# Optimization experiments

Measured on AMD Instinct MI355X. Metric: run time of the kernel, lower is better.

The kernel has to match this reference:

```python
import jax, jax.numpy as jnp
import numpy as np

HEADS = 4
HEAD_DIM = 32
DIM = 256
HIDDEN = HEADS * HEAD_DIM  # 128
SCALE = HEAD_DIM ** -0.5


def rmsnorm(x, g):
    # channel-wise L2 normalize (dim=1) * g * sqrt(C), lucidrains-style RMSNorm for conv maps
    inv = jax.lax.rsqrt(jnp.sum(x * x, axis=1, keepdims=True) + 1e-12)
    return x * inv * (g * (x.shape[1] ** 0.5))[None, :, None, None]


def setup_inputs() -> dict:
    key = jax.random.key(0)
    k1, k2, k3 = jax.random.split(key, 3)
    b, H, W = 16, 64, 64
    x = jax.random.normal(k1, (b, DIM, H, W), dtype=jnp.float32)
    W_qkv = jax.random.normal(k2, (3 * HIDDEN, DIM), dtype=jnp.float32) * (DIM ** -0.5)
    W_out = jax.random.normal(k3, (DIM, HIDDEN), dtype=jnp.float32) * (HIDDEN ** -0.5)
    b_out = jnp.zeros((DIM,), dtype=jnp.float32)
    g_norm = jnp.ones((DIM,), dtype=jnp.float32)
    g_out = jnp.ones((DIM,), dtype=jnp.float32)
    return {"x": x, "W_qkv": W_qkv, "W_out": W_out, "b_out": b_out,
            "g_norm": g_norm, "g_out": g_out}


def reference(x, W_qkv, W_out, b_out, g_norm, g_out):
    b, c, H, W = x.shape
    n = H * W
    xn = rmsnorm(x, g_norm)
    # 1x1 conv projection to q,k,v: (b, 3*hidden, H, W)
    qkv = jnp.einsum('bchw,oc->bohw', xn, W_qkv)
    qkv = qkv.reshape(b, 3, HEADS, HEAD_DIM, n)
    q, k, v = qkv[:, 0], qkv[:, 1], qkv[:, 2]  # (b, h, d, n)
    q = jax.nn.softmax(q, axis=-2)  # over head_dim
    k = jax.nn.softmax(k, axis=-1)  # over tokens
    # context: (b, h, d, e)
    context = jnp.einsum('bhdn,bhen->bhde', k, v)
    out = jnp.einsum('bhde,bhdn->bhen', context, q) * SCALE  # (b, h, e, n)
    out = out.reshape(b, HIDDEN, H, W)
    out = jnp.einsum('bchw,oc->bohw', out, W_out) + b_out[None, :, None, None]
    return rmsnorm(out, g_out)
```

## Files before the change

### kernel.cpp

```cpp
#include <hip/hip_runtime.h>


typedef _Float16 half8 __attribute__((ext_vector_type(8)));
typedef _Float16 half4 __attribute__((ext_vector_type(4)));
typedef float f32x4 __attribute__((ext_vector_type(4)));

#define SCALE_F 0.17677669529663687f

__global__ __launch_bounds__(256) void kW(const float* __restrict__ W_qkv,
                                          const float* __restrict__ W_out,
                                          const float* __restrict__ g_norm,
                                          _Float16* __restrict__ W16,
                                          _Float16* __restrict__ Wo16) {
  const int t = threadIdx.x;
  __shared__ float g16s[256];
  g16s[t] = g_norm[t] * 16.0f;
  __syncthreads();
  #pragma unroll
  for (int i = 0; i < 8; ++i) {
    int idx = blockIdx.x * 2048 + i * 256 + t;
    if (idx < 24576) {
      f32x4 v = *(const f32x4*)(W_qkv + (size_t)idx * 4);
      int c0 = (idx & 63) * 4;
      half4 h = {(_Float16)(v[0] * g16s[c0]), (_Float16)(v[1] * g16s[c0 + 1]),
                 (_Float16)(v[2] * g16s[c0 + 2]), (_Float16)(v[3] * g16s[c0 + 3])};
      *(half4*)(W16 + (size_t)idx * 4) = h;
    } else {
      f32x4 v = *(const f32x4*)(W_out + (size_t)(idx - 24576) * 4);
      half4 h = {(_Float16)v[0], (_Float16)v[1], (_Float16)v[2], (_Float16)v[3]};
      *(half4*)(Wo16 + (size_t)(idx - 24576) * 4) = h;
    }
  }
}

#define LOAD_AF(dst, mtv)                                                            \
  {                                                                                  \
    const _Float16* Wm_ = W16 + (size_t)((mtv) * 128 + h * 32) * 256;                \
    _Pragma("unroll")                                                                \
    for (int ks = 0; ks < 8; ++ks)                                                   \
      _Pragma("unroll")                                                              \
      for (int mf = 0; mf < 2; ++mf)                                                 \
        dst[ks][mf] = *(const half8*)(Wm_ + (size_t)(mf * 16 + ll) * 256 +           \
                                      ks * 32 + lg * 8);                             \
  }

#define GEMM_PHASE(afc)                                                              \
  {                                                                                  \
    _Pragma("unroll")                                                                \
    for (int i = 0; i < 2; ++i)                                                      \
      _Pragma("unroll")                                                              \
      for (int j = 0; j < 4; ++j) acc[i][j] = fz;                                    \
    _Pragma("unroll")                                                                \
    for (int ks = 0; ks < 8; ++ks) {                                                 \
      half8 bf[4];                                                                   \
      _Pragma("unroll")                                                              \
      for (int nf = 0; nf < 4; ++nf)                                                 \
        bf[nf] = *(const half8*)(xbuf + (nf * 16 + ll) * 512 +                       \
                                 ((((ks * 4 + lg) ^ ll) ^ ((nf & 1) << 4)) << 4));   \
      _Pragma("unroll")                                                              \
      for (int mf = 0; mf < 2; ++mf)                                                 \
        _Pragma("unroll")                                                            \
        for (int nf = 0; nf < 4; ++nf)                                               \
          acc[mf][nf] =                                                              \
              __builtin_amdgcn_mfma_f32_16x16x32_f16(afc[ks][mf], bf[nf],            \
                                                     acc[mf][nf], 0, 0, 0);          \
    }                                                                                \
  }

__global__ __launch_bounds__(256, 3) void k2_mega(const _Float16* __restrict__ W16,
                                                  const float* __restrict__ x,
                                                  _Float16* __restrict__ qhat,
                                                  float* __restrict__ ctxp,
                                                  float* __restrict__ sumep) {
  const int pt = blockIdx.x, b = blockIdx.y;
  const int p0 = pt * 64;
  const int t = threadIdx.x;
  const int h = t >> 6, l = t & 63;
  const int lg = l >> 4, ll = l & 15;
  const int u = l & 3;
  __shared__ __align__(1024) char smem[50176];
  char* xbuf = smem;
  char* wt = smem + 32768;
  char* vt = smem;
  float* psum = (float*)(smem + 49152);

  f32x4 vx[16];
  const float* xb = x + ((size_t)(b * 256 + h * 64)) * 4096 + p0 + (l & ~3);
  #pragma unroll
  for (int it = 0; it < 16; ++it)
    vx[it] = *(const f32x4*)(xb + (size_t)(it * 4 + u) * 4096);
  half8 afA[8][2], afB[8][2];
  LOAD_AF(afA, 0);
  float rsum = 0.f;
  #pragma unroll
  for (int it = 0; it < 16; ++it) {
    f32x4 v = vx[it];
    float sA = __shfl_xor((u & 1) ? v[0] : v[1], 1);
    float sB = __shfl_xor((u & 1) ? v[2] : v[3], 1);
    float a0 = (u & 1) ? sA : v[0];
    float a1 = (u & 1) ? v[1] : sA;
    float a2 = (u & 1) ? sB : v[2];
    float a3 = (u & 1) ? v[3] : sB;
    float sC = __shfl_xor((u & 2) ? a0 : a2, 2);
    float sD = __shfl_xor((u & 2) ? a1 : a3, 2);
    float w0 = (u & 2) ? sC : a0;
    float w1 = (u & 2) ? sD : a1;
    float w2 = (u & 2) ? a2 : sC;
    float w3 = (u & 2) ? a3 : sD;
    half4 hv = {(_Float16)w0, (_Float16)w1, (_Float16)w2, (_Float16)w3};
    #pragma unroll
    for (int j = 0; j < 4; ++j) { float f = (float)hv[j]; rsum += f * f; }
    int c = h * 8 + (it >> 1);
    int swz = c ^ (l & 15) ^ (((l >> 4) & 1) << 4);
    *(half4*)(xbuf + l * 512 + (swz << 4) + (it & 1) * 8) = hv;
  }
  psum[l * 4 + h] = rsum;
  __syncthreads();
  float sv[4];
  #pragma unroll
  for (int nf = 0; nf < 4; ++nf) {
    int px = nf * 16 + ll;
    sv[nf] = rsqrtf(psum[px * 4] + psum[px * 4 + 1] + psum[px * 4 + 2] +
                    psum[px * 4 + 3] + 1e-12f);
  }

  const f32x4 fz = {0.f, 0.f, 0.f, 0.f};
  f32x4 acc[2][4];

  GEMM_PHASE(afA);
  LOAD_AF(afB, 1);
  {
    float s[4] = {0.f, 0.f, 0.f, 0.f};
    #pragma unroll
    for (int mf = 0; mf < 2; ++mf)
      #pragma unroll
      for (int nf = 0; nf < 4; ++nf)
        #pragma unroll
        for (int rr = 0; rr < 4; ++rr) {
          float v = __expf(acc[mf][nf][rr] * sv[nf]);
          acc[mf][nf][rr] = v;
          s[nf] += v;
        }
    #pragma unroll
    for (int nf = 0; nf < 4; ++nf) {
      s[nf] += __shfl_xor(s[nf], 16);
      s[nf] += __shfl_xor(s[nf], 32);
      s[nf] = 1.0f / s[nf];
    }
    _Float16* qb = qhat + ((size_t)b * 4096 + p0) * 128 + h * 32 + lg * 4;
    #pragma unroll
    for (int mf = 0; mf < 2; ++mf)
      #pragma unroll
      for (int nf = 0; nf < 4; ++nf) {
        int px = nf * 16 + ll;
        half4 hv;
        #pragma unroll
        for (int rr = 0; rr < 4; ++rr) hv[rr] = (_Float16)(acc[mf][nf][rr] * s[nf]);
        *(half4*)(qb + (size_t)px * 128 + mf * 16) = hv;
      }
  }

  GEMM_PHASE(afB);
  LOAD_AF(afA, 2);
  {
    float rs[2][4];
    #pragma unroll
    for (int mf = 0; mf < 2; ++mf)
      #pragma unroll
      for (int rr = 0; rr < 4; ++rr) rs[mf][rr] = 0.f;
    #pragma unroll
    for (int mf = 0; mf < 2; ++mf)
      #pragma unroll
      for (int nf = 0; nf < 4; ++nf)
        #pragma unroll
        for (int rr = 0; rr < 4; ++rr) {
          float v = __expf(acc[mf][nf][rr] * sv[nf] - 10.f);
          acc[mf][nf][rr] = v;
          rs[mf][rr] += v;
        }
    #pragma unroll
    for (int mf = 0; mf < 2; ++mf)
      #pragma unroll
      for (int rr = 0; rr < 4; ++rr) {
        float v = rs[mf][rr];
        v += __shfl_xor(v, 1);
        v += __shfl_xor(v, 2);
        v += __shfl_xor(v, 4);
        v += __shfl_xor(v, 8);
        rs[mf][rr] = v;
      }
    if (ll == 0) {
      #pragma unroll
      for (int mf = 0; mf < 2; ++mf)
        #pragma unroll
        for (int rr = 0; rr < 4; ++rr)
          sumep[((size_t)b * 128 + h * 32 + mf * 16 + lg * 4 + rr) * 64 + pt] = rs[mf][rr];
    }
    #pragma unroll
    for (int mf = 0; mf < 2; ++mf)
      #pragma unroll
      for (int nf = 0; nf < 4; ++nf)
        #pragma unroll
        for (int rr = 0; rr < 4; ++rr) {
          int ch = h * 32 + mf * 16 + lg * 4 + rr;
          int px = nf * 16 + ll;
          *(_Float16*)(wt + ch * 128 + (((px >> 3) ^ (ch & 7)) << 4) + (px & 7) * 2) =
              (_Float16)acc[mf][nf][rr];
        }
  }

  GEMM_PHASE(afA);
  {
    __syncthreads();
    #pragma unroll
    for (int mf = 0; mf < 2; ++mf)
      #pragma unroll
      for (int nf = 0; nf < 4; ++nf)
        #pragma unroll
        for (int rr = 0; rr < 4; ++rr) {
          int ch = h * 32 + mf * 16 + lg * 4 + rr;
          int px = nf * 16 + ll;
          *(_Float16*)(vt + ch * 128 + (((px >> 3) ^ (ch & 7)) << 4) + (px & 7) * 2) =
              (_Float16)(acc[mf][nf][rr] * sv[nf]);
        }
    f32x4 ca[2][2] = {{fz, fz}, {fz, fz}};
    #pragma unroll
    for (int ks2 = 0; ks2 < 2; ++ks2) {
      half8 a2[2], b2[2];
      #pragma unroll
      for (int ti = 0; ti < 2; ++ti) {
        int ra = h * 32 + ti * 16 + ll;
        int cc = (ks2 * 4 + lg) ^ (ra & 7);
        a2[ti] = *(const half8*)(wt + ra * 128 + (cc << 4));
        b2[ti] = *(const half8*)(vt + ra * 128 + (cc << 4));
      }
      #pragma unroll
      for (int ti = 0; ti < 2; ++ti)
        #pragma unroll
        for (int tj = 0; tj < 2; ++tj)
          ca[ti][tj] = __builtin_amdgcn_mfma_f32_16x16x32_f16(a2[ti], b2[tj], ca[ti][tj], 0, 0, 0);
    }
    float* cp = ctxp + (size_t)(((b * 64 + pt) * 4) + h) * 1024;
    #pragma unroll
    for (int ti = 0; ti < 2; ++ti)
      #pragma unroll
      for (int tj = 0; tj < 2; ++tj)
        #pragma unroll
        for (int rr = 0; rr < 4; ++rr)
          cp[(ti * 16 + lg * 4 + rr) * 32 + tj * 16 + ll] = ca[ti][tj][rr];
  }
}

__global__ __launch_bounds__(256) void k34(const float* __restrict__ ctxp,
                                           const float* __restrict__ sumep,
                                           const _Float16* __restrict__ Wo16,
                                           _Float16* __restrict__ M) {
  const int h = blockIdx.x, b = blockIdx.y;
  const int t = threadIdx.x;
  __shared__ float ctx_s[1024];
  __shared__ float sis[32];
  {
    f32x4 a = {0.f, 0.f, 0.f, 0.f};
    const float* p = ctxp + ((size_t)(b * 64) * 4 + h) * 1024 + t * 4;
    #pragma unroll 8
    for (int pt = 0; pt < 64; ++pt) {
      f32x4 v = *(const f32x4*)(p + (size_t)pt * 4096);
      a[0] += v[0]; a[1] += v[1]; a[2] += v[2]; a[3] += v[3];
    }
    *(f32x4*)(ctx_s + t * 4) = a;
  }
  if (t < 32) {
    float s = 0.f;
    const float* sp = sumep + ((size_t)b * 128 + h * 32 + t) * 64;
    #pragma unroll 8
    for (int pt = 0; pt < 64; ++pt) s += sp[pt];
    sis[t] = SCALE_F / s;
  }
  __syncthreads();
  const int w = t >> 6, l = t & 63;
  const int m0 = w * 64;
  half8 bf[2];
  #pragma unroll
  for (int n0 = 0; n0 < 2; ++n0) {
    int d = n0 * 16 + (l & 15);
    float s = sis[d];
    const float* ce = ctx_s + d * 32 + (l >> 4) * 8;
    half8 hb;
    #pragma unroll
    for (int j = 0; j < 8; ++j) hb[j] = (_Float16)(ce[j] * s);
    bf[n0] = hb;
  }
  const f32x4 fz = {0.f, 0.f, 0.f, 0.f};
  _Float16* Mb = M + (size_t)(b * 256) * 128;
  #pragma unroll
  for (int mf = 0; mf < 4; ++mf) {
    int row = m0 + mf * 16 + (l & 15);
    half8 af = *(const half8*)(Wo16 + (size_t)row * 128 + h * 32 + (l >> 4) * 8);
    #pragma unroll
    for (int n0 = 0; n0 < 2; ++n0) {
      f32x4 c = __builtin_amdgcn_mfma_f32_16x16x32_f16(af, bf[n0], fz, 0, 0, 0);
      #pragma unroll
      for (int rr = 0; rr < 4; ++rr) {
        int r = m0 + mf * 16 + (l >> 4) * 4 + rr;
        Mb[(size_t)r * 128 + h * 32 + n0 * 16 + (l & 15)] = (_Float16)c[rr];
      }
    }
  }
}

__global__ __launch_bounds__(256) void k5c_out(const _Float16* __restrict__ M,
                                               const _Float16* __restrict__ qhat,
                                               const float* __restrict__ b_out,
                                               const float* __restrict__ g_out,
                                               float* __restrict__ out) {
  const int pt = blockIdx.x, b = blockIdx.y;
  const int p0 = pt * 64;
  const int t = threadIdx.x;
  const int wid = t >> 6, l = t & 63;
  __shared__ __align__(16) char smem[81920];
  float* rp = (float*)smem;
  float* bo = (float*)(smem + 69632);
  float* g16o = (float*)(smem + 70656);
  float* psum = (float*)(smem + 71680);
  float* sinvp = (float*)(smem + 72704);
  const _Float16* Mb = M + (size_t)b * 256 * 128;
  const _Float16* Qb = qhat + ((size_t)b * 4096 + p0) * 128;
  #pragma unroll
  for (int i = 0; i < 16; ++i) {
    int ci = t + 256 * i;
    int r = ci >> 4, c = ci & 15;
    *(half8*)(smem + r * 256 + ((c ^ (r & 15)) << 4)) = *(const half8*)(Mb + (size_t)r * 128 + c * 8);
  }
  #pragma unroll
  for (int i = 0; i < 4; ++i) {
    int ci = t + 256 * i;
    int r = ci >> 4, c = ci & 15;
    *(half8*)(smem + 65536 + r * 256 + ((c ^ (r & 15)) << 4)) = *(const half8*)(Qb + (size_t)r * 128 + c * 8);
  }
  __syncthreads();
  const f32x4 fz = {0.f, 0.f, 0.f, 0.f};
  f32x4 acc[4][4];
  #pragma unroll
  for (int i = 0; i < 4; ++i)
    #pragma unroll
    for (int j = 0; j < 4; ++j) acc[i][j] = fz;
  #pragma unroll
  for (int kk = 0; kk < 4; ++kk) {
    half8 af[4], bf[4];
    int ck = kk * 4 + (l >> 4);
    #pragma unroll
    for (int mf = 0; mf < 4; ++mf) {
      int r = wid * 64 + mf * 16 + (l & 15);
      af[mf] = *(const half8*)(smem + r * 256 + ((ck ^ (r & 15)) << 4));
    }
    #pragma unroll
    for (int nf = 0; nf < 4; ++nf) {
      int r = nf * 16 + (l & 15);
      bf[nf] = *(const half8*)(smem + 65536 + r * 256 + ((ck ^ (r & 15)) << 4));
    }
    #pragma unroll
    for (int mf = 0; mf < 4; ++mf)
      #pragma unroll
      for (int nf = 0; nf < 4; ++nf)
        acc[mf][nf] = __builtin_amdgcn_mfma_f32_16x16x32_f16(af[mf], bf[nf], acc[mf][nf], 0, 0, 0);
  }
  __syncthreads();
  bo[t] = b_out[t];
  g16o[t] = g_out[t] * 16.0f;
  #pragma unroll
  for (int mf = 0; mf < 4; ++mf)
    #pragma unroll
    for (int nf = 0; nf < 4; ++nf)
      #pragma unroll
      for (int rr = 0; rr < 4; ++rr) {
        int r = wid * 64 + mf * 16 + (l >> 4) * 4 + rr;
        int px = nf * 16 + (l & 15);
        rp[r * 68 + px] = acc[mf][nf][rr];
      }
  __syncthreads();
  {
    int px = t & 63, q = t >> 6;
    float s = 0.f;
    #pragma unroll
    for (int i = 0; i < 64; ++i) {
      int r = q * 64 + i;
      float f = rp[r * 68 + px] + bo[r];
      s += f * f;
    }
    psum[px * 4 + q] = s;
  }
  __syncthreads();
  if (t < 64)
    sinvp[t] = rsqrtf(psum[t * 4] + psum[t * 4 + 1] + psum[t * 4 + 2] + psum[t * 4 + 3] + 1e-12f);
  __syncthreads();
  float* ob = out + (size_t)(b * 256) * 4096 + p0;
  #pragma unroll
  for (int i = 0; i < 16; ++i) {
    int idx4 = t + 256 * i;
    int r = idx4 >> 4, px4 = (idx4 & 15) * 4;
    f32x4 v;
    #pragma unroll
    for (int ii = 0; ii < 4; ++ii)
      v[ii] = (rp[r * 68 + px4 + ii] + bo[r]) * sinvp[px4 + ii] * g16o[r];
    *(f32x4*)(ob + (size_t)r * 4096 + px4) = v;
  }
}

extern "C" void kernel_launch(void* const* d_in, const int* in_sizes, int n_in,
                              void* d_out, int out_size, void* d_ws, size_t ws_size,
                              hipStream_t stream) {
  const float* x      = (const float*)d_in[0];
  const float* W_qkv  = (const float*)d_in[1];
  const float* W_out  = (const float*)d_in[2];
  const float* b_out  = (const float*)d_in[3];
  const float* g_norm = (const float*)d_in[4];
  const float* g_out  = (const float*)d_in[5];
  float* out = (float*)d_out;
  char* ws = (char*)d_ws;
  if (ws_size < 35659776) return;

  _Float16* W16   = (_Float16*)(ws);
  _Float16* Wo16  = (_Float16*)(ws + 196608);
  _Float16* qhat  = (_Float16*)(ws + 262144);
  _Float16* M     = (_Float16*)(ws + 17039360);
  float*    ctxp  = (float*)(ws + 18358272);
  float*    sumep = (float*)(ws + 35135488);

  kW<<<16, 256, 0, stream>>>(W_qkv, W_out, g_norm, W16, Wo16);
  k2_mega<<<dim3(64, 16), 256, 0, stream>>>(W16, x, qhat, ctxp, sumep);
  k34<<<dim3(4, 16), 256, 0, stream>>>(ctxp, sumep, Wo16, M);
  k5c_out<<<dim3(64, 16), 256, 0, stream>>>(M, qhat, b_out, g_out, out);
}
```

Before: 78.86 us.

## Fuse QKV projections into one K-loop and stage q output through LDS

Replaces three sequential GEMM phases, each holding a full preloaded weight fragment set in registers, with a single K-loop that computes q, k and v accumulators together, reusing each x fragment load across all three. The q softmax output is now written to a swizzled LDS tile and copied out with coalesced 16-byte global stores instead of scattered 8-byte stores. The LDS layout is reorganised so v gets its own region, and launch bounds drop to 2 blocks per CU to fit the larger accumulator state. It trades occupancy and register pressure for fewer LDS reads and better global store coalescing.

Result: no change. 79.95 us (+1.4%).

```diff
diff --git a/kernel.cpp b/kernel.cpp
--- a/kernel.cpp
+++ b/kernel.cpp
@@ -33,41 +33,7 @@
   }
 }
 
-#define LOAD_AF(dst, mtv)                                                            \
-  {                                                                                  \
-    const _Float16* Wm_ = W16 + (size_t)((mtv) * 128 + h * 32) * 256;                \
-    _Pragma("unroll")                                                                \
-    for (int ks = 0; ks < 8; ++ks)                                                   \
-      _Pragma("unroll")                                                              \
-      for (int mf = 0; mf < 2; ++mf)                                                 \
-        dst[ks][mf] = *(const half8*)(Wm_ + (size_t)(mf * 16 + ll) * 256 +           \
-                                      ks * 32 + lg * 8);                             \
-  }
-
-#define GEMM_PHASE(afc)                                                              \
-  {                                                                                  \
-    _Pragma("unroll")                                                                \
-    for (int i = 0; i < 2; ++i)                                                      \
-      _Pragma("unroll")                                                              \
-      for (int j = 0; j < 4; ++j) acc[i][j] = fz;                                    \
-    _Pragma("unroll")                                                                \
-    for (int ks = 0; ks < 8; ++ks) {                                                 \
-      half8 bf[4];                                                                   \
-      _Pragma("unroll")                                                              \
-      for (int nf = 0; nf < 4; ++nf)                                                 \
-        bf[nf] = *(const half8*)(xbuf + (nf * 16 + ll) * 512 +                       \
-                                 ((((ks * 4 + lg) ^ ll) ^ ((nf & 1) << 4)) << 4));   \
-      _Pragma("unroll")                                                              \
-      for (int mf = 0; mf < 2; ++mf)                                                 \
-        _Pragma("unroll")                                                            \
-        for (int nf = 0; nf < 4; ++nf)                                               \
-          acc[mf][nf] =                                                              \
-              __builtin_amdgcn_mfma_f32_16x16x32_f16(afc[ks][mf], bf[nf],            \
-                                                     acc[mf][nf], 0, 0, 0);          \
-    }                                                                                \
-  }
-
-__global__ __launch_bounds__(256, 3) void k2_mega(const _Float16* __restrict__ W16,
+__global__ __launch_bounds__(256, 2) void k2_mega(const _Float16* __restrict__ W16,
                                                   const float* __restrict__ x,
                                                   _Float16* __restrict__ qhat,
                                                   float* __restrict__ ctxp,
@@ -80,8 +46,9 @@
   const int u = l & 3;
   __shared__ __align__(1024) char smem[50176];
   char* xbuf = smem;
+  char* qt = smem;
+  char* vt = smem + 16384;
   char* wt = smem + 32768;
-  char* vt = smem;
   float* psum = (float*)(smem + 49152);
 
   f32x4 vx[16];
@@ -89,8 +56,6 @@
   #pragma unroll
   for (int it = 0; it < 16; ++it)
     vx[it] = *(const f32x4*)(xb + (size_t)(it * 4 + u) * 4096);
-  half8 afA[8][2], afB[8][2];
-  LOAD_AF(afA, 0);
   float rsum = 0.f;
   #pragma unroll
   for (int it = 0; it < 16; ++it) {
@@ -125,10 +90,38 @@
   }
 
   const f32x4 fz = {0.f, 0.f, 0.f, 0.f};
-  f32x4 acc[2][4];
-
-  GEMM_PHASE(afA);
-  LOAD_AF(afB, 1);
+  f32x4 acc[3][2][4];
+  #pragma unroll
+  for (int mt = 0; mt < 3; ++mt)
+    #pragma unroll
+    for (int i = 0; i < 2; ++i)
+      #pragma unroll
+      for (int j = 0; j < 4; ++j) acc[mt][i][j] = fz;
+  #pragma unroll
+  for (int ks = 0; ks < 8; ++ks) {
+    half8 bf[4];
+    #pragma unroll
+    for (int nf = 0; nf < 4; ++nf)
+      bf[nf] = *(const half8*)(xbuf + (nf * 16 + ll) * 512 +
+                               ((((ks * 4 + lg) ^ ll) ^ ((nf & 1) << 4)) << 4));
+    half8 afl[3][2];
+    #pragma unroll
+    for (int mt = 0; mt < 3; ++mt)
+      #pragma unroll
+      for (int mf = 0; mf < 2; ++mf)
+        afl[mt][mf] = *(const half8*)(W16 +
+            (size_t)(mt * 128 + h * 32 + mf * 16 + ll) * 256 + ks * 32 + lg * 8);
+    #pragma unroll
+    for (int mt = 0; mt < 3; ++mt)
+      #pragma unroll
+      for (int mf = 0; mf < 2; ++mf)
+        #pragma unroll
+        for (int nf = 0; nf < 4; ++nf)
+          acc[mt][mf][nf] = __builtin_amdgcn_mfma_f32_16x16x32_f16(
+              afl[mt][mf], bf[nf], acc[mt][mf][nf], 0, 0, 0);
+  }
+  __syncthreads();
+
   {
     float s[4] = {0.f, 0.f, 0.f, 0.f};
     #pragma unroll
@@ -137,8 +130,8 @@
       for (int nf = 0; nf < 4; ++nf)
         #pragma unroll
         for (int rr = 0; rr < 4; ++rr) {
-          float v = __expf(acc[mf][nf][rr] * sv[nf]);
-          acc[mf][nf][rr] = v;
+          float v = __expf(acc[0][mf][nf][rr] * sv[nf]);
+          acc[0][mf][nf][rr] = v;
           s[nf] += v;
         }
     #pragma unroll
@@ -147,21 +140,30 @@
       s[nf] += __shfl_xor(s[nf], 32);
       s[nf] = 1.0f / s[nf];
     }
-    _Float16* qb = qhat + ((size_t)b * 4096 + p0) * 128 + h * 32 + lg * 4;
     #pragma unroll
     for (int mf = 0; mf < 2; ++mf)
       #pragma unroll
       for (int nf = 0; nf < 4; ++nf) {
         int px = nf * 16 + ll;
+        int cphys = (h * 4 + mf * 2 + (lg >> 1)) ^ (px & 15);
         half4 hv;
         #pragma unroll
-        for (int rr = 0; rr < 4; ++rr) hv[rr] = (_Float16)(acc[mf][nf][rr] * s[nf]);
-        *(half4*)(qb + (size_t)px * 128 + mf * 16) = hv;
+        for (int rr = 0; rr < 4; ++rr) hv[rr] = (_Float16)(acc[0][mf][nf][rr] * s[nf]);
+        *(half4*)(qt + px * 256 + (cphys << 4) + (lg & 1) * 8) = hv;
       }
   }
-
-  GEMM_PHASE(afB);
-  LOAD_AF(afA, 2);
+  __syncthreads();
+  {
+    _Float16* qb = qhat + ((size_t)b * 4096 + p0) * 128;
+    #pragma unroll
+    for (int i = 0; i < 4; ++i) {
+      int q = i * 256 + t;
+      int px = q >> 4, g = q & 15;
+      half8 hv = *(const half8*)(qt + px * 256 + ((g ^ (px & 15)) << 4));
+      *(half8*)(qb + (size_t)px * 128 + g * 8) = hv;
+    }
+  }
+
   {
     float rs[2][4];
     #pragma unroll
@@ -174,8 +176,8 @@
       for (int nf = 0; nf < 4; ++nf)
         #pragma unroll
         for (int rr = 0; rr < 4; ++rr) {
-          float v = __expf(acc[mf][nf][rr] * sv[nf] - 10.f);
-          acc[mf][nf][rr] = v;
+          float v = __expf(acc[1][mf][nf][rr] * sv[nf] - 10.f);
+          acc[1][mf][nf][rr] = v;
           rs[mf][rr] += v;
         }
     #pragma unroll
@@ -205,13 +207,11 @@
           int ch = h * 32 + mf * 16 + lg * 4 + rr;
           int px = nf * 16 + ll;
           *(_Float16*)(wt + ch * 128 + (((px >> 3) ^ (ch & 7)) << 4) + (px & 7) * 2) =
-              (_Float16)acc[mf][nf][rr];
+              (_Float16)acc[1][mf][nf][rr];
         }
   }
 
-  GEMM_PHASE(afA);
-  {
-    __syncthreads();
+  {
     #pragma unroll
     for (int mf = 0; mf < 2; ++mf)
       #pragma unroll
@@ -221,7 +221,7 @@
           int ch = h * 32 + mf * 16 + lg * 4 + rr;
           int px = nf * 16 + ll;
           *(_Float16*)(vt + ch * 128 + (((px >> 3) ^ (ch & 7)) << 4) + (px & 7) * 2) =
-              (_Float16)(acc[mf][nf][rr] * sv[nf]);
+              (_Float16)(acc[2][mf][nf][rr] * sv[nf]);
         }
     f32x4 ca[2][2] = {{fz, fz}, {fz, fz}};
     #pragma unroll
```
